# Performance work log

Measured on AMD Instinct MI355X. Metric: run time of the kernel, lower is better.

The kernel has to match this reference:

```python
import jax, jax.numpy as jnp
import numpy as np
from jax import lax

H = 64  # hidden_size

def _lstm_layer(x, w_ih, w_hh, b_ih, b_hh):
    # x: (B, T, in). PyTorch gate order [i, f, g, o]; gates = x@W_ih^T + h@W_hh^T + b_ih + b_hh.
    B, T, _ = x.shape
    xw = jnp.einsum('bti,gi->btg', x, w_ih) + (b_ih + b_hh)  # (B, T, 4H), input projection hoisted out of scan

    def step(carry, xw_t):
        h, c = carry
        gates = xw_t + h @ w_hh.T                     # (B, 4H)
        i, f, g, o = jnp.split(gates, 4, axis=-1)
        i = jax.nn.sigmoid(i)
        f = jax.nn.sigmoid(f)
        g = jnp.tanh(g)
        o = jax.nn.sigmoid(o)
        c = f * c + i * g
        h = o * jnp.tanh(c)
        return (h, c), h

    h0 = jnp.zeros((B, H), dtype=x.dtype)
    c0 = jnp.zeros((B, H), dtype=x.dtype)
    (h_n, _), hs = lax.scan(step, (h0, c0), jnp.swapaxes(xw, 0, 1))  # hs: (T, B, H)
    return jnp.swapaxes(hs, 0, 1), h_n


def setup_inputs() -> dict:
    key = jax.random.key(0)
    ks = jax.random.split(key, 12)
    s = 1.0 / np.sqrt(H)  # PyTorch LSTM init scale
    return {
        'x':     jax.random.normal(ks[0], (2048, 512, 4), dtype=jnp.float32),
        'w_ih0': jax.random.uniform(ks[1], (4 * H, 4), jnp.float32, -s, s),
        'w_hh0': jax.random.uniform(ks[2], (4 * H, H), jnp.float32, -s, s),
        'b_ih0': jax.random.uniform(ks[3], (4 * H,), jnp.float32, -s, s),
        'b_hh0': jax.random.uniform(ks[4], (4 * H,), jnp.float32, -s, s),
        'w_ih1': jax.random.uniform(ks[5], (4 * H, H), jnp.float32, -s, s),
        'w_hh1': jax.random.uniform(ks[6], (4 * H, H), jnp.float32, -s, s),
        'b_ih1': jax.random.uniform(ks[7], (4 * H,), jnp.float32, -s, s),
        'b_hh1': jax.random.uniform(ks[8], (4 * H,), jnp.float32, -s, s),
        'fc_w':  jax.random.uniform(ks[9], (H, H), jnp.float32, -s, s),
        'fc_b':  jax.random.uniform(ks[10], (H,), jnp.float32, -s, s),
    }


def reference(x, w_ih0, w_hh0, b_ih0, b_hh0, w_ih1, w_hh1, b_ih1, b_hh1, fc_w, fc_b):
    # 2-layer LSTM (eval mode: inter-layer dropout inactive), take last layer's final hidden,
    # then Linear + tanh.
    h1_seq, _ = _lstm_layer(x, w_ih0, w_hh0, b_ih0, b_hh0)
    _, h_n = _lstm_layer(h1_seq, w_ih1, w_hh1, b_ih1, b_hh1)
    return jnp.tanh(h_n @ fc_w.T + fc_b)
```

## Files before the change

### kernel.cpp

```cpp
#include <hip/hip_runtime.h>


#define HID 64
#define TSTEPS 512
#define MB 8
#define BLK 512
#define HSTR 88
#define LOG2E  1.4426950408889634f
#define LOG2E2 2.8853900817779268f

typedef _Float16 f16;
typedef _Float16 half8 __attribute__((ext_vector_type(8)));
typedef _Float16 half4 __attribute__((ext_vector_type(4)));
typedef float f32x4 __attribute__((ext_vector_type(4)));

__device__ __forceinline__ float tanh2(float y) {
    return fmaf(2.0f, __builtin_amdgcn_rcpf(1.0f + __builtin_amdgcn_exp2f(-y)), -1.0f);
}

__global__ __launch_bounds__(BLK, 2) void lstm_mfma(
    const float* __restrict__ x,
    const float* __restrict__ w_ih0,
    const float* __restrict__ w_hh0,
    const float* __restrict__ b_ih0,
    const float* __restrict__ b_hh0,
    const float* __restrict__ w_ih1,
    const float* __restrict__ w_hh1,
    const float* __restrict__ b_ih1,
    const float* __restrict__ b_hh1,
    const float* __restrict__ fc_w,
    const float* __restrict__ fc_b,
    float* __restrict__ out)
{
    __shared__ f16 xs[TSTEPS * MB * 4];
    __shared__ f16 h0s[2][MB * HSTR];
    __shared__ f16 h1s[2][MB * HSTR];

    const int tid  = threadIdx.x;
    const int w    = tid >> 6;
    const int l    = tid & 63;
    const int quad = l >> 4;
    const int l15  = l & 15;
    const int wl   = w & 3;
    const bool isL0 = (w < 4);
    const int b0   = blockIdx.x * MB;

    const int RM = (l15 < 8) ? l15 : ((l15 & 4) | ((l15 + 2) & 3));

    for (int it = tid; it < MB * TSTEPS; it += BLK) {
        const int m = it >> 9;
        const int t = it & 511;
        const float4 v = *((const float4*)x + (size_t)(b0 + m) * TSTEPS + t);
        *(half4*)(xs + (t * MB + m) * 4) =
            (half4){ (f16)v.x, (f16)v.y, (f16)v.z, (f16)v.w };
    }
    for (int it = tid; it < MB * HSTR; it += BLK) {
        h0s[0][it] = (f16)0.f; h0s[1][it] = (f16)0.f;
        h1s[0][it] = (f16)0.f; h1s[1][it] = (f16)0.f;
    }

    half8 Bf[4][4];
    f32x4 biasv[4];
    const half8 Z = { (f16)0.f,(f16)0.f,(f16)0.f,(f16)0.f,
                      (f16)0.f,(f16)0.f,(f16)0.f,(f16)0.f };
    #pragma unroll
    for (int ti = 0; ti < 4; ++ti) {
        const int n = (wl + 4 * ti) * 16 + l15;
        const float sc = (ti == 2) ? LOG2E2 : LOG2E;
        float bval;
        if (isL0) {
            bval = (b_ih0[n] + b_hh0[n]) * sc;
            half8 pz = Z;
            if (quad == 0) {
                const float4 v = *(const float4*)(w_ih0 + n * 4);
                pz[0] = (f16)(v.x * sc); pz[1] = (f16)(v.y * sc);
                pz[2] = (f16)(v.z * sc); pz[3] = (f16)(v.w * sc);
            }
            Bf[ti][0] = pz;
            #pragma unroll
            for (int ks = 0; ks < 2; ++ks) {
                const int ko = ks * 32 + quad * 8;
                const float4 a = *(const float4*)(w_hh0 + n * HID + ko);
                const float4 b = *(const float4*)(w_hh0 + n * HID + ko + 4);
                Bf[ti][1 + ks] = (half8){
                    (f16)(a.x*sc),(f16)(a.y*sc),(f16)(a.z*sc),(f16)(a.w*sc),
                    (f16)(b.x*sc),(f16)(b.y*sc),(f16)(b.z*sc),(f16)(b.w*sc) };
            }
            Bf[ti][3] = Z;
        } else {
            bval = (b_ih1[n] + b_hh1[n]) * sc;
            #pragma unroll
            for (int ks = 0; ks < 2; ++ks) {
                const int ko = ks * 32 + quad * 8;
                const float4 a = *(const float4*)(w_ih1 + n * HID + ko);
                const float4 b = *(const float4*)(w_ih1 + n * HID + ko + 4);
                Bf[ti][ks] = (half8){
                    (f16)(a.x*sc),(f16)(a.y*sc),(f16)(a.z*sc),(f16)(a.w*sc),
                    (f16)(b.x*sc),(f16)(b.y*sc),(f16)(b.z*sc),(f16)(b.w*sc) };
                const float4 c = *(const float4*)(w_hh1 + n * HID + ko);
                const float4 d = *(const float4*)(w_hh1 + n * HID + ko + 4);
                Bf[ti][2 + ks] = (half8){
                    (f16)(c.x*sc),(f16)(c.y*sc),(f16)(c.z*sc),(f16)(c.w*sc),
                    (f16)(d.x*sc),(f16)(d.y*sc),(f16)(d.z*sc),(f16)(d.w*sc) };
            }
        }
        biasv[ti] = (f32x4){ bval, bval, bval, bval };
    }

    const int  mrow = (quad & 1) * 4 + (quad & 2);
    const int  uu   = wl * 16 + l15;
    const int  hb   = RM * HSTR + quad * 8;
    float cst0 = 0.f, cst1 = 0.f;
    f32x4 g[4];

    auto load_x = [&](int r) -> half4 {
        return *(const half4*)(xs + (r * MB + RM) * 4);
    };
    auto l0_mfma = [&](half4 xv, const f16* h0rd) {
        __builtin_amdgcn_s_setprio(1);
        half8 ax = Z;
        if (quad == 0) { ax[0]=xv[0]; ax[1]=xv[1]; ax[2]=xv[2]; ax[3]=xv[3]; }
        const half8 A1 = *(const half8*)(h0rd + hb);
        const half8 A2 = *(const half8*)(h0rd + hb + 32);
        #pragma unroll
        for (int ti = 0; ti < 4; ++ti) {
            f32x4 acc;
            acc   = __builtin_amdgcn_mfma_f32_16x16x32_f16(ax, Bf[ti][0], biasv[ti], 0, 0, 0);
            acc   = __builtin_amdgcn_mfma_f32_16x16x32_f16(A1, Bf[ti][1], acc, 0, 0, 0);
            g[ti] = __builtin_amdgcn_mfma_f32_16x16x32_f16(A2, Bf[ti][2], acc, 0, 0, 0);
        }
        __builtin_amdgcn_s_setprio(0);
    };
    auto l1_mfma = [&](const f16* h0rd, const f16* h1rd) {
        const half8 A1 = *(const half8*)(h0rd + hb);
        const half8 A2 = *(const half8*)(h0rd + hb + 32);
        const half8 A3 = *(const half8*)(h1rd + hb);
        const half8 A4 = *(const half8*)(h1rd + hb + 32);
        #pragma unroll
        for (int ti = 0; ti < 4; ++ti) {
            f32x4 acc;
            acc   = __builtin_amdgcn_mfma_f32_16x16x32_f16(A1, Bf[ti][0], biasv[ti], 0, 0, 0);
            acc   = __builtin_amdgcn_mfma_f32_16x16x32_f16(A2, Bf[ti][1], acc, 0, 0, 0);
            acc   = __builtin_amdgcn_mfma_f32_16x16x32_f16(A3, Bf[ti][2], acc, 0, 0, 0);
            g[ti] = __builtin_amdgcn_mfma_f32_16x16x32_f16(A4, Bf[ti][3], acc, 0, 0, 0);
        }
    };
    auto act_store = [&](f16* dst) {
        #pragma unroll
        for (int j = 0; j < 2; ++j) {
            const float ei = __builtin_amdgcn_exp2f(-g[0][j]);
            const float ef = __builtin_amdgcn_exp2f(-g[1][j]);
            const float eg = __builtin_amdgcn_exp2f(-g[2][j]);
            const float eo = __builtin_amdgcn_exp2f(-g[3][j]);
            float& c = j ? cst1 : cst0;
            const float af = 1.0f + ef;
            const float P  = (1.0f + ei) * (1.0f + eg);
            const float N  = fmaf(c * P, 1.0f, (1.0f - eg) * af);
            c = N * __builtin_amdgcn_rcpf(P * af);
            const float ym = fminf(-LOG2E2 * c, 126.0f);
            const float ec = __builtin_amdgcn_exp2f(ym);
            const float r2 = __builtin_amdgcn_rcpf((1.0f + eo) * (1.0f + ec));
            dst[(mrow + j) * HSTR + uu] = (f16)((1.0f - ec) * r2);
        }
    };

    __syncthreads();

    half4 xv;
    if (isL0) xv = load_x(0);
    if (isL0) { l0_mfma(xv, h0s[1]); act_store(h0s[0]); xv = load_x(1); }
    __syncthreads();
    if (isL0) { l0_mfma(xv, h0s[0]); act_store(h0s[1]); xv = load_x(2); }
    else      { l1_mfma(h0s[0], h1s[1]); act_store(h1s[0]); }
    __syncthreads();

    #pragma unroll 1
    for (int r = 2; r < 510; r += 2) {
        if (isL0) { l0_mfma(xv, h0s[1]); act_store(h0s[0]); xv = load_x(r + 1); }
        else      { l1_mfma(h0s[1], h1s[0]); act_store(h1s[1]); }
        __syncthreads();
        if (isL0) { l0_mfma(xv, h0s[0]); act_store(h0s[1]); xv = load_x(r + 2); }
        else      { l1_mfma(h0s[0], h1s[1]); act_store(h1s[0]); }
        __syncthreads();
    }
    if (isL0) { l0_mfma(xv, h0s[1]); act_store(h0s[0]); xv = load_x(511); }
    else      { l1_mfma(h0s[1], h1s[0]); act_store(h1s[1]); }
    __syncthreads();
    if (isL0) { l0_mfma(xv, h0s[0]); act_store(h0s[1]); }
    else      { l1_mfma(h0s[0], h1s[1]); act_store(h1s[0]); }
    __syncthreads();
    if (!isL0) { l1_mfma(h0s[1], h1s[0]); act_store(h1s[1]); }
    __syncthreads();

    {
        const int v = tid & 63;
        const int m = tid >> 6;
        float a = fc_b[v];
        const f16* hp = h1s[1] + m * HSTR;
        const float4* wp = (const float4*)(fc_w + v * HID);
        #pragma unroll
        for (int kk = 0; kk < HID / 4; ++kk) {
            const float4 wv = wp[kk];
            a += (float)hp[kk * 4 + 0] * wv.x + (float)hp[kk * 4 + 1] * wv.y
               + (float)hp[kk * 4 + 2] * wv.z + (float)hp[kk * 4 + 3] * wv.w;
        }
        out[(size_t)(b0 + m) * HID + v] = tanh2(a * LOG2E2);
    }
}

extern "C" void kernel_launch(void* const* d_in, const int* in_sizes, int n_in,
                              void* d_out, int out_size, void* d_ws, size_t ws_size,
                              hipStream_t stream) {
    const float* x     = (const float*)d_in[0];
    const float* w_ih0 = (const float*)d_in[1];
    const float* w_hh0 = (const float*)d_in[2];
    const float* b_ih0 = (const float*)d_in[3];
    const float* b_hh0 = (const float*)d_in[4];
    const float* w_ih1 = (const float*)d_in[5];
    const float* w_hh1 = (const float*)d_in[6];
    const float* b_ih1 = (const float*)d_in[7];
    const float* b_hh1 = (const float*)d_in[8];
    const float* fc_w  = (const float*)d_in[9];
    const float* fc_b  = (const float*)d_in[10];
    float* out = (float*)d_out;

    const int B = in_sizes[0] / (TSTEPS * 4);
    lstm_mfma<<<dim3(B / MB), dim3(BLK), 0, stream>>>(
        x, w_ih0, w_hh0, b_ih0, b_hh0, w_ih1, w_hh1, b_ih1, b_hh1, fc_w, fc_b, out);
}
```

Measured before the change: 327.2 us.

## Replace block barriers with LDS counter spin-waits between LSTM layer waves

Drops the per-step __syncthreads lockstep between layer-0 and layer-1 waves. Instead, shared-memory counters signal when each wave has finished a step, so layer 0 can run up to three steps ahead of layer 1. The h0 history buffer grows to four slots to make that possible, and layer-1 MFMA sections also get raised wave priority. In exchange, waves spin on volatile LDS reads and rely on acquire/release fences for correctness, so wasted issue slots or ordering bugs are possible.

```diff
diff --git a/kernel.cpp b/kernel.cpp
--- a/kernel.cpp
+++ b/kernel.cpp
@@ -33,8 +33,10 @@
     float* __restrict__ out)
 {
     __shared__ f16 xs[TSTEPS * MB * 4];
-    __shared__ f16 h0s[2][MB * HSTR];
+    __shared__ f16 h0s[4][MB * HSTR];
     __shared__ f16 h1s[2][MB * HSTR];
+    __shared__ int prod0;
+    __shared__ int prod1;
 
     const int tid  = threadIdx.x;
     const int w    = tid >> 6;
@@ -56,8 +58,10 @@
     }
     for (int it = tid; it < MB * HSTR; it += BLK) {
         h0s[0][it] = (f16)0.f; h0s[1][it] = (f16)0.f;
+        h0s[2][it] = (f16)0.f; h0s[3][it] = (f16)0.f;
         h1s[0][it] = (f16)0.f; h1s[1][it] = (f16)0.f;
     }
+    if (tid == 0) { prod0 = 0; prod1 = 0; }
 
     half8 Bf[4][4];
     f32x4 biasv[4];
@@ -116,6 +120,15 @@
     auto load_x = [&](int r) -> half4 {
         return *(const half4*)(xs + (r * MB + RM) * 4);
     };
+    auto spin_ge = [&](int* p, int target) {
+        volatile int* vp = (volatile int*)p;
+        while (*vp < target) {}
+        __builtin_amdgcn_fence(__ATOMIC_ACQUIRE, "workgroup");
+    };
+    auto done = [&](int* p) {
+        __builtin_amdgcn_fence(__ATOMIC_RELEASE, "workgroup");
+        if (l == 0) atomicAdd(p, 1);
+    };
     auto l0_mfma = [&](half4 xv, const f16* h0rd) {
         __builtin_amdgcn_s_setprio(1);
         half8 ax = Z;
@@ -132,6 +145,7 @@
         __builtin_amdgcn_s_setprio(0);
     };
     auto l1_mfma = [&](const f16* h0rd, const f16* h1rd) {
+        __builtin_amdgcn_s_setprio(1);
         const half8 A1 = *(const half8*)(h0rd + hb);
         const half8 A2 = *(const half8*)(h0rd + hb + 32);
         const half8 A3 = *(const half8*)(h1rd + hb);
@@ -144,6 +158,7 @@
             acc   = __builtin_amdgcn_mfma_f32_16x16x32_f16(A3, Bf[ti][2], acc, 0, 0, 0);
             g[ti] = __builtin_amdgcn_mfma_f32_16x16x32_f16(A4, Bf[ti][3], acc, 0, 0, 0);
         }
+        __builtin_amdgcn_s_setprio(0);
     };
     auto act_store = [&](f16* dst) {
         #pragma unroll
@@ -166,30 +181,28 @@
 
     __syncthreads();
 
-    half4 xv;
-    if (isL0) xv = load_x(0);
-    if (isL0) { l0_mfma(xv, h0s[1]); act_store(h0s[0]); xv = load_x(1); }
-    __syncthreads();
-    if (isL0) { l0_mfma(xv, h0s[0]); act_store(h0s[1]); xv = load_x(2); }
-    else      { l1_mfma(h0s[0], h1s[1]); act_store(h1s[0]); }
-    __syncthreads();
-
-    #pragma unroll 1
-    for (int r = 2; r < 510; r += 2) {
-        if (isL0) { l0_mfma(xv, h0s[1]); act_store(h0s[0]); xv = load_x(r + 1); }
-        else      { l1_mfma(h0s[1], h1s[0]); act_store(h1s[1]); }
-        __syncthreads();
-        if (isL0) { l0_mfma(xv, h0s[0]); act_store(h0s[1]); xv = load_x(r + 2); }
-        else      { l1_mfma(h0s[0], h1s[1]); act_store(h1s[0]); }
-        __syncthreads();
-    }
-    if (isL0) { l0_mfma(xv, h0s[1]); act_store(h0s[0]); xv = load_x(511); }
-    else      { l1_mfma(h0s[1], h1s[0]); act_store(h1s[1]); }
-    __syncthreads();
-    if (isL0) { l0_mfma(xv, h0s[0]); act_store(h0s[1]); }
-    else      { l1_mfma(h0s[0], h1s[1]); act_store(h1s[0]); }
-    __syncthreads();
-    if (!isL0) { l1_mfma(h0s[1], h1s[0]); act_store(h1s[1]); }
+    if (isL0) {
+        half4 xv = load_x(0);
+        #pragma unroll 1
+        for (int r = 0; r < TSTEPS; ++r) {
+            spin_ge(&prod0, 4 * r);
+            l0_mfma(xv, h0s[(r + 3) & 3]);
+            xv = load_x((r + 1) & 511);
+            spin_ge(&prod1, 4 * (r - 3));
+            act_store(h0s[r & 3]);
+            done(&prod0);
+        }
+    } else {
+        #pragma unroll 1
+        for (int s = 0; s < TSTEPS; ++s) {
+            spin_ge(&prod1, 4 * s);
+            spin_ge(&prod0, 4 * (s + 1));
+            l1_mfma(h0s[s & 3], h1s[(s + 1) & 1]);
+            act_store(h1s[s & 1]);
+            done(&prod1);
+        }
+    }
+
     __syncthreads();
 
     {
```

Result: slower. 379.5 us (+16.0%).

## Stagger layer-0 and layer-1 warps so MFMA and activation phases alternate

Applied to the files above, without the earlier changes.

Each timestep is split into two barrier-separated phases. In the first phase the layer-0 waves run their matrix products while the layer-1 waves run activations and stores; in the second phase the roles swap. The aim is to keep the matrix units and the transcendental/VALU units busy at the same time instead of every wave contending for the same unit at once. The h1 state is reduced to a single buffer, and layer-1 matrix products now also get raised wave priority. The cost is twice as many block barriers per timestep, and the wave-group schedule becomes more fragile.

```diff
diff --git a/kernel.cpp b/kernel.cpp
--- a/kernel.cpp
+++ b/kernel.cpp
@@ -34,7 +34,7 @@
 {
     __shared__ f16 xs[TSTEPS * MB * 4];
     __shared__ f16 h0s[2][MB * HSTR];
-    __shared__ f16 h1s[2][MB * HSTR];
+    __shared__ f16 h1s[MB * HSTR];
 
     const int tid  = threadIdx.x;
     const int w    = tid >> 6;
@@ -56,7 +56,7 @@
     }
     for (int it = tid; it < MB * HSTR; it += BLK) {
         h0s[0][it] = (f16)0.f; h0s[1][it] = (f16)0.f;
-        h1s[0][it] = (f16)0.f; h1s[1][it] = (f16)0.f;
+        h1s[it] = (f16)0.f;
     }
 
     half8 Bf[4][4];
@@ -132,6 +132,7 @@
         __builtin_amdgcn_s_setprio(0);
     };
     auto l1_mfma = [&](const f16* h0rd, const f16* h1rd) {
+        __builtin_amdgcn_s_setprio(1);
         const half8 A1 = *(const half8*)(h0rd + hb);
         const half8 A2 = *(const half8*)(h0rd + hb + 32);
         const half8 A3 = *(const half8*)(h1rd + hb);
@@ -144,6 +145,7 @@
             acc   = __builtin_amdgcn_mfma_f32_16x16x32_f16(A3, Bf[ti][2], acc, 0, 0, 0);
             g[ti] = __builtin_amdgcn_mfma_f32_16x16x32_f16(A4, Bf[ti][3], acc, 0, 0, 0);
         }
+        __builtin_amdgcn_s_setprio(0);
     };
     auto act_store = [&](f16* dst) {
         #pragma unroll
@@ -168,35 +170,37 @@
 
     half4 xv;
     if (isL0) xv = load_x(0);
-    if (isL0) { l0_mfma(xv, h0s[1]); act_store(h0s[0]); xv = load_x(1); }
+
+    #pragma unroll 1
+    for (int r = 0; r < TSTEPS; ++r) {
+        if (isL0) {
+            l0_mfma(xv, h0s[(r + 1) & 1]);
+            xv = load_x((r + 1) & 511);
+        } else if (r >= 2) {
+            act_store(h1s);
+        }
+        __syncthreads();
+        if (isL0) {
+            act_store(h0s[r & 1]);
+        } else if (r >= 1) {
+            l1_mfma(h0s[(r + 1) & 1], h1s);
+        }
+        __syncthreads();
+    }
+
+    if (!isL0) act_store(h1s);
     __syncthreads();
-    if (isL0) { l0_mfma(xv, h0s[0]); act_store(h0s[1]); xv = load_x(2); }
-    else      { l1_mfma(h0s[0], h1s[1]); act_store(h1s[0]); }
-    __syncthreads();
-
-    #pragma unroll 1
-    for (int r = 2; r < 510; r += 2) {
-        if (isL0) { l0_mfma(xv, h0s[1]); act_store(h0s[0]); xv = load_x(r + 1); }
-        else      { l1_mfma(h0s[1], h1s[0]); act_store(h1s[1]); }
-        __syncthreads();
-        if (isL0) { l0_mfma(xv, h0s[0]); act_store(h0s[1]); xv = load_x(r + 2); }
-        else      { l1_mfma(h0s[0], h1s[1]); act_store(h1s[0]); }
-        __syncthreads();
-    }
-    if (isL0) { l0_mfma(xv, h0s[1]); act_store(h0s[0]); xv = load_x(511); }
-    else      { l1_mfma(h0s[1], h1s[0]); act_store(h1s[1]); }
-    __syncthreads();
-    if (isL0) { l0_mfma(xv, h0s[0]); act_store(h0s[1]); }
-    else      { l1_mfma(h0s[0], h1s[1]); act_store(h1s[0]); }
-    __syncthreads();
-    if (!isL0) { l1_mfma(h0s[1], h1s[0]); act_store(h1s[1]); }
+    if (!isL0) {
+        l1_mfma(h0s[1], h1s);
+        act_store(h1s);
+    }
     __syncthreads();
 
     {
         const int v = tid & 63;
         const int m = tid >> 6;
         float a = fc_b[v];
-        const f16* hp = h1s[1] + m * HSTR;
+        const f16* hp = h1s + m * HSTR;
         const float4* wp = (const float4*)(fc_w + v * HID);
         #pragma unroll
         for (int kk = 0; kk < HID / 4; ++kk) {
```

Result: slower. 394.7 us (+20.6%).

## Merge layer 0 and layer 1 into same waves with software-pipelined schedule

Applied to the files above, without the earlier changes.

Instead of splitting the block into four layer-0 waves and four layer-1 waves, each of four waves now computes both layers. The schedule interleaves layer-1 activation of step r-2 with layer-0 MFMAs of step r, and layer-0 activation with layer-1 MFMAs, using a 4-deep h0 ring buffer. The aim is for transcendental work and matrix work to overlap within a wave while the block size halves. Register pressure roughly doubles (both weight sets held per lane) and the launch bounds drop to one block per SIMD, which changes occupancy.

```diff
diff --git a/kernel.cpp b/kernel.cpp
--- a/kernel.cpp
+++ b/kernel.cpp
@@ -4,7 +4,7 @@
 #define HID 64
 #define TSTEPS 512
 #define MB 8
-#define BLK 512
+#define BLK 256
 #define HSTR 88
 #define LOG2E  1.4426950408889634f
 #define LOG2E2 2.8853900817779268f
@@ -18,7 +18,7 @@
     return fmaf(2.0f, __builtin_amdgcn_rcpf(1.0f + __builtin_amdgcn_exp2f(-y)), -1.0f);
 }
 
-__global__ __launch_bounds__(BLK, 2) void lstm_mfma(
+__global__ __launch_bounds__(BLK, 1) void lstm_mfma(
     const float* __restrict__ x,
     const float* __restrict__ w_ih0,
     const float* __restrict__ w_hh0,
@@ -33,16 +33,14 @@
     float* __restrict__ out)
 {
     __shared__ f16 xs[TSTEPS * MB * 4];
-    __shared__ f16 h0s[2][MB * HSTR];
+    __shared__ f16 h0s[4][MB * HSTR];
     __shared__ f16 h1s[2][MB * HSTR];
 
     const int tid  = threadIdx.x;
-    const int w    = tid >> 6;
+    const int wl   = tid >> 6;
     const int l    = tid & 63;
     const int quad = l >> 4;
     const int l15  = l & 15;
-    const int wl   = w & 3;
-    const bool isL0 = (w < 4);
     const int b0   = blockIdx.x * MB;
 
     const int RM = (l15 < 8) ? l15 : ((l15 & 4) | ((l15 + 2) & 3));
@@ -56,103 +54,98 @@
     }
     for (int it = tid; it < MB * HSTR; it += BLK) {
         h0s[0][it] = (f16)0.f; h0s[1][it] = (f16)0.f;
+        h0s[2][it] = (f16)0.f; h0s[3][it] = (f16)0.f;
         h1s[0][it] = (f16)0.f; h1s[1][it] = (f16)0.f;
     }
 
-    half8 Bf[4][4];
-    f32x4 biasv[4];
+    half8 B0[4][3];
+    half8 B1[4][4];
+    f32x4 bias0[4], bias1[4];
     const half8 Z = { (f16)0.f,(f16)0.f,(f16)0.f,(f16)0.f,
                       (f16)0.f,(f16)0.f,(f16)0.f,(f16)0.f };
     #pragma unroll
     for (int ti = 0; ti < 4; ++ti) {
         const int n = (wl + 4 * ti) * 16 + l15;
         const float sc = (ti == 2) ? LOG2E2 : LOG2E;
-        float bval;
-        if (isL0) {
-            bval = (b_ih0[n] + b_hh0[n]) * sc;
+        {
+            const float bval = (b_ih0[n] + b_hh0[n]) * sc;
             half8 pz = Z;
             if (quad == 0) {
                 const float4 v = *(const float4*)(w_ih0 + n * 4);
                 pz[0] = (f16)(v.x * sc); pz[1] = (f16)(v.y * sc);
                 pz[2] = (f16)(v.z * sc); pz[3] = (f16)(v.w * sc);
             }
-            Bf[ti][0] = pz;
+            B0[ti][0] = pz;
             #pragma unroll
             for (int ks = 0; ks < 2; ++ks) {
                 const int ko = ks * 32 + quad * 8;
                 const float4 a = *(const float4*)(w_hh0 + n * HID + ko);
                 const float4 b = *(const float4*)(w_hh0 + n * HID + ko + 4);
-                Bf[ti][1 + ks] = (half8){
+                B0[ti][1 + ks] = (half8){
                     (f16)(a.x*sc),(f16)(a.y*sc),(f16)(a.z*sc),(f16)(a.w*sc),
                     (f16)(b.x*sc),(f16)(b.y*sc),(f16)(b.z*sc),(f16)(b.w*sc) };
             }
-            Bf[ti][3] = Z;
-        } else {
-            bval = (b_ih1[n] + b_hh1[n]) * sc;
+            bias0[ti] = (f32x4){ bval, bval, bval, bval };
+        }
+        {
+            const float bval = (b_ih1[n] + b_hh1[n]) * sc;
             #pragma unroll
             for (int ks = 0; ks < 2; ++ks) {
                 const int ko = ks * 32 + quad * 8;
                 const float4 a = *(const float4*)(w_ih1 + n * HID + ko);
                 const float4 b = *(const float4*)(w_ih1 + n * HID + ko + 4);
-                Bf[ti][ks] = (half8){
+                B1[ti][ks] = (half8){
                     (f16)(a.x*sc),(f16)(a.y*sc),(f16)(a.z*sc),(f16)(a.w*sc),
                     (f16)(b.x*sc),(f16)(b.y*sc),(f16)(b.z*sc),(f16)(b.w*sc) };
                 const float4 c = *(const float4*)(w_hh1 + n * HID + ko);
                 const float4 d = *(const float4*)(w_hh1 + n * HID + ko + 4);
-                Bf[ti][2 + ks] = (half8){
+                B1[ti][2 + ks] = (half8){
                     (f16)(c.x*sc),(f16)(c.y*sc),(f16)(c.z*sc),(f16)(c.w*sc),
                     (f16)(d.x*sc),(f16)(d.y*sc),(f16)(d.z*sc),(f16)(d.w*sc) };
             }
-        }
-        biasv[ti] = (f32x4){ bval, bval, bval, bval };
+            bias1[ti] = (f32x4){ bval, bval, bval, bval };
+        }
     }
 
     const int  mrow = (quad & 1) * 4 + (quad & 2);
     const int  uu   = wl * 16 + l15;
     const int  hb   = RM * HSTR + quad * 8;
-    float cst0 = 0.f, cst1 = 0.f;
-    f32x4 g[4];
+    float c00 = 0.f, c01 = 0.f;
+    float c10 = 0.f, c11 = 0.f;
+    f32x4 g0[4], g1[4];
 
     auto load_x = [&](int r) -> half4 {
         return *(const half4*)(xs + (r * MB + RM) * 4);
     };
-    auto l0_mfma = [&](half4 xv, const f16* h0rd) {
-        __builtin_amdgcn_s_setprio(1);
+    auto l0_mfma = [&](half4 xv, half8 A1, half8 A2) {
         half8 ax = Z;
         if (quad == 0) { ax[0]=xv[0]; ax[1]=xv[1]; ax[2]=xv[2]; ax[3]=xv[3]; }
-        const half8 A1 = *(const half8*)(h0rd + hb);
-        const half8 A2 = *(const half8*)(h0rd + hb + 32);
         #pragma unroll
         for (int ti = 0; ti < 4; ++ti) {
             f32x4 acc;
-            acc   = __builtin_amdgcn_mfma_f32_16x16x32_f16(ax, Bf[ti][0], biasv[ti], 0, 0, 0);
-            acc   = __builtin_amdgcn_mfma_f32_16x16x32_f16(A1, Bf[ti][1], acc, 0, 0, 0);
-            g[ti] = __builtin_amdgcn_mfma_f32_16x16x32_f16(A2, Bf[ti][2], acc, 0, 0, 0);
-        }
-        __builtin_amdgcn_s_setprio(0);
-    };
-    auto l1_mfma = [&](const f16* h0rd, const f16* h1rd) {
-        const half8 A1 = *(const half8*)(h0rd + hb);
-        const half8 A2 = *(const half8*)(h0rd + hb + 32);
-        const half8 A3 = *(const half8*)(h1rd + hb);
-        const half8 A4 = *(const half8*)(h1rd + hb + 32);
+            acc    = __builtin_amdgcn_mfma_f32_16x16x32_f16(ax, B0[ti][0], bias0[ti], 0, 0, 0);
+            acc    = __builtin_amdgcn_mfma_f32_16x16x32_f16(A1, B0[ti][1], acc, 0, 0, 0);
+            g0[ti] = __builtin_amdgcn_mfma_f32_16x16x32_f16(A2, B0[ti][2], acc, 0, 0, 0);
+        }
+    };
+    auto l1_mfma = [&](half8 A1, half8 A2, half8 A3, half8 A4) {
         #pragma unroll
         for (int ti = 0; ti < 4; ++ti) {
             f32x4 acc;
-            acc   = __builtin_amdgcn_mfma_f32_16x16x32_f16(A1, Bf[ti][0], biasv[ti], 0, 0, 0);
-            acc   = __builtin_amdgcn_mfma_f32_16x16x32_f16(A2, Bf[ti][1], acc, 0, 0, 0);
-            acc   = __builtin_amdgcn_mfma_f32_16x16x32_f16(A3, Bf[ti][2], acc, 0, 0, 0);
-            g[ti] = __builtin_amdgcn_mfma_f32_16x16x32_f16(A4, Bf[ti][3], acc, 0, 0, 0);
-        }
-    };
-    auto act_store = [&](f16* dst) {
+            acc    = __builtin_amdgcn_mfma_f32_16x16x32_f16(A1, B1[ti][0], bias1[ti], 0, 0, 0);
+            acc    = __builtin_amdgcn_mfma_f32_16x16x32_f16(A2, B1[ti][1], acc, 0, 0, 0);
+            acc    = __builtin_amdgcn_mfma_f32_16x16x32_f16(A3, B1[ti][2], acc, 0, 0, 0);
+            g1[ti] = __builtin_amdgcn_mfma_f32_16x16x32_f16(A4, B1[ti][3], acc, 0, 0, 0);
+        }
+    };
+    auto act_store = [&](const f32x4* gg, f16* dst, float& ca, float& cb) {
         #pragma unroll
         for (int j = 0; j < 2; ++j) {
-            const float ei = __builtin_amdgcn_exp2f(-g[0][j]);
-            const float ef = __builtin_amdgcn_exp2f(-g[1][j]);
-            const float eg = __builtin_amdgcn_exp2f(-g[2][j]);
-            const float eo = __builtin_amdgcn_exp2f(-g[3][j]);
-            float& c = j ? cst1 : cst0;
+            const float ei = __builtin_amdgcn_exp2f(-gg[0][j]);
+            const float ef = __builtin_amdgcn_exp2f(-gg[1][j]);
+            const float eg = __builtin_amdgcn_exp2f(-gg[2][j]);
+            const float eo = __builtin_amdgcn_exp2f(-gg[3][j]);
+            float& c = j ? cb : ca;
             const float af = 1.0f + ef;
             const float P  = (1.0f + ei) * (1.0f + eg);
             const float N  = fmaf(c * P, 1.0f, (1.0f - eg) * af);
@@ -166,35 +159,41 @@
 
     __syncthreads();
 
-    half4 xv;
-    if (isL0) xv = load_x(0);
-    if (isL0) { l0_mfma(xv, h0s[1]); act_store(h0s[0]); xv = load_x(1); }
+    half4 xv = load_x(0);
+
+    #pragma unroll 1
+    for (int r = 0; r < TSTEPS; ++r) {
+        const f16* h0rd = h0s[(r + 3) & 3];
+        const half8 A1 = *(const half8*)(h0rd + hb);
+        const half8 A2 = *(const half8*)(h0rd + hb + 32);
+        if (r >= 2) act_store(g1, h1s[r & 1], c10, c11);
+        l0_mfma(xv, A1, A2);
+        __syncthreads();
+        const f16* h1rd = h1s[r & 1];
+        const half8 A3 = *(const half8*)(h1rd + hb);
+        const half8 A4 = *(const half8*)(h1rd + hb + 32);
+        act_store(g0, h0s[r & 3], c00, c01);
+        l1_mfma(A1, A2, A3, A4);
+        xv = load_x((r + 1) & 511);
+        __syncthreads();
+    }
+
+    act_store(g1, h1s[0], c10, c11);
     __syncthreads();
-    if (isL0) { l0_mfma(xv, h0s[0]); act_store(h0s[1]); xv = load_x(2); }
-    else      { l1_mfma(h0s[0], h1s[1]); act_store(h1s[0]); }
+    {
+        const f16* h0rd = h0s[3];
+        const half8 A1 = *(const half8*)(h0rd + hb);
+        const half8 A2 = *(const half8*)(h0rd + hb + 32);
+        const half8 A3 = *(const half8*)(h1s[0] + hb);
+        const half8 A4 = *(const half8*)(h1s[0] + hb + 32);
+        l1_mfma(A1, A2, A3, A4);
+        act_store(g1, h1s[1], c10, c11);
+    }
     __syncthreads();
 
-    #pragma unroll 1
-    for (int r = 2; r < 510; r += 2) {
-        if (isL0) { l0_mfma(xv, h0s[1]); act_store(h0s[0]); xv = load_x(r + 1); }
-        else      { l1_mfma(h0s[1], h1s[0]); act_store(h1s[1]); }
-        __syncthreads();
-        if (isL0) { l0_mfma(xv, h0s[0]); act_store(h0s[1]); xv = load_x(r + 2); }
-        else      { l1_mfma(h0s[0], h1s[1]); act_store(h1s[0]); }
-        __syncthreads();
-    }
-    if (isL0) { l0_mfma(xv, h0s[1]); act_store(h0s[0]); xv = load_x(511); }
-    else      { l1_mfma(h0s[1], h1s[0]); act_store(h1s[1]); }
-    __syncthreads();
-    if (isL0) { l0_mfma(xv, h0s[0]); act_store(h0s[1]); }
-    else      { l1_mfma(h0s[0], h1s[1]); act_store(h1s[0]); }
-    __syncthreads();
-    if (!isL0) { l1_mfma(h0s[1], h1s[0]); act_store(h1s[1]); }
-    __syncthreads();
-
-    {
-        const int v = tid & 63;
-        const int m = tid >> 6;
+    for (int it = tid; it < MB * HID; it += BLK) {
+        const int v = it & 63;
+        const int m = it >> 6;
         float a = fc_b[v];
         const f16* hp = h1s[1] + m * HSTR;
         const float4* wp = (const float4*)(fc_w + v * HID);
```

Result: slower. 368.1 us (+12.5%).
